# Kernel tuning notes

Measured on AMD Instinct MI355X. Metric: run time of the kernel, lower is better.

Reference implementation:

```python
import jax, jax.numpy as jnp
import numpy as np

B, S, H = 2, 4096, 2048
NH, NKV, HD = 16, 4, 128          # heads, kv heads, head_dim = H // NH
GS_RATIO = 0.25                    # hardcoded in MyAttention.forward
ROPE_BASE = 10000.0


def rotate_half(x):
    h = x.shape[-1] // 2
    return jnp.concatenate((-x[..., h:], x[..., :h]), axis=-1)


def setup_inputs() -> dict:
    key = jax.random.key(0)
    ks = jax.random.split(key, 5)
    g = int(S * GS_RATIO)
    hidden_states = jax.random.normal(ks[0], (B, S, H), jnp.float32)
    position_ids = jnp.tile(jnp.arange(S, dtype=jnp.int32)[None, :], (B, 1))
    # causal additive mask per group window (0 keep, -1e9 masked)
    i = jnp.arange(g)
    causal = i[None, :] <= i[:, None]
    attention_mask = jnp.broadcast_to(
        jnp.where(causal, 0.0, -1e9).astype(jnp.float32)[None, None], (B, 1, g, g)
    )
    sc = 0.02
    Wq = (jax.random.normal(ks[1], (H, NH * HD), jnp.float32) * sc)
    Wk = (jax.random.normal(ks[2], (H, NKV * HD), jnp.float32) * sc)
    Wv = (jax.random.normal(ks[3], (H, NKV * HD), jnp.float32) * sc)
    Wo = (jax.random.normal(ks[4], (NH * HD, H), jnp.float32) * sc)
    return {"hidden_states": hidden_states, "attention_mask": attention_mask,
            "position_ids": position_ids, "Wq": Wq, "Wk": Wk, "Wv": Wv, "Wo": Wo}


def reference(hidden_states, attention_mask, position_ids, Wq, Wk, Wv, Wo):
    B_, S_, H_ = hidden_states.shape
    g = int(S_ * GS_RATIO)
    ng = S_ // g
    n_rep = NH // NKV

    # QKV projections -> (B, heads, S, HD)
    q = (hidden_states @ Wq).reshape(B_, S_, NH, HD).transpose(0, 2, 1, 3)
    k = (hidden_states @ Wk).reshape(B_, S_, NKV, HD).transpose(0, 2, 1, 3)
    v = (hidden_states @ Wv).reshape(B_, S_, NKV, HD).transpose(0, 2, 1, 3)

    # RoPE
    inv_freq = 1.0 / (ROPE_BASE ** (jnp.arange(0, HD, 2, dtype=jnp.float32) / HD))
    t = jnp.arange(S_, dtype=jnp.float32)
    emb = jnp.concatenate([jnp.outer(t, inv_freq)] * 2, axis=-1)  # (S, HD)
    cos = jnp.cos(emb)[position_ids][:, None]  # (B,1,S,HD)
    sin = jnp.sin(emb)[position_ids][:, None]
    q = q * cos + rotate_half(q) * sin
    k = k * cos + rotate_half(k) * sin

    # GQA repeat_kv
    k = jnp.repeat(k, n_rep, axis=1)
    v = jnp.repeat(v, n_rep, axis=1)

    # S2-Attn shift: roll second half of heads by -g/2 along seq, then group
    def shift(x):
        x = jnp.concatenate([x[:, :NH // 2],
                             jnp.roll(x[:, NH // 2:], -g // 2, axis=2)], axis=1)
        return x.transpose(0, 2, 1, 3).reshape(B_ * ng, g, NH, HD).transpose(0, 2, 1, 3)

    q, k, v = shift(q), shift(k), shift(v)

    attn = jnp.einsum('bhqd,bhkd->bhqk', q, k) / np.float32(np.sqrt(HD))
    mask = jnp.tile(attention_mask, (ng, 1, 1, 1))  # (B*ng,1,g,g)
    attn = attn + mask
    attn = jax.nn.softmax(attn.astype(jnp.float32), axis=-1).astype(q.dtype)

    out = jnp.einsum('bhqk,bhkd->bhqd', attn, v)  # (B*ng, NH, g, HD)
    out = out.transpose(0, 2, 1, 3).reshape(B_, S_, NH, HD)
    # undo shift for second half of heads (+g/2 along seq)
    out = jnp.concatenate([out[:, :, :NH // 2],
                           jnp.roll(out[:, :, NH // 2:], g // 2, axis=1)], axis=2)
    out = out.reshape(B_, S_, NH * HD) @ Wo
    return out
```

## Files before the change

kernel.cpp:

```cpp
#include <hip/hip_runtime.h>
#include <math.h>

typedef unsigned short u16;
typedef short bf16x8 __attribute__((ext_vector_type(8)));
typedef float f32x4 __attribute__((ext_vector_type(4)));


__device__ __forceinline__ u16 f2bf(float x) {
  union { float f; unsigned u; } c; c.f = x;
  unsigned r = (c.u + 0x7FFFu + ((c.u >> 16) & 1u)) >> 16;
  return (u16)r;
}
__device__ __forceinline__ float bf2f(u16 x) {
  union { unsigned u; float f; } c; c.u = ((unsigned)x) << 16;
  return c.f;
}

#define GLD16(gp, lp)                                                   \
  __builtin_amdgcn_global_load_lds(                                     \
      (__attribute__((address_space(1))) void*)(gp),                    \
      (__attribute__((address_space(3))) void*)(lp), 16, 0, 0)

#define WAITVM(n) asm volatile("s_waitcnt vmcnt(" #n ")" ::: "memory")
#define LGKM0 { asm volatile("s_waitcnt lgkmcnt(0)" ::: "memory"); \
                __builtin_amdgcn_sched_barrier(0); }
#define BARF  { __builtin_amdgcn_s_barrier(); asm volatile("" ::: "memory"); }

__global__ __launch_bounds__(256) void cast_bf16_vec(
    const float* __restrict__ X, u16* __restrict__ Y) {
  const size_t i = ((size_t)blockIdx.x * 256 + threadIdx.x) * 4;
  float4 v = *(const float4*)(X + i);
  ushort4 o;
  o.x = f2bf(v.x); o.y = f2bf(v.y); o.z = f2bf(v.z); o.w = f2bf(v.w);
  *(ushort4*)(Y + i) = o;
}

__global__ __launch_bounds__(256) void wt_cast(
    const float* __restrict__ W, u16* __restrict__ Wt, int K, int N) {
  const int bk = blockIdx.y * 64;
  const int bn = blockIdx.x * 64;
  __shared__ float T[64 * 65];
  const int tid = threadIdx.x;
  #pragma unroll
  for (int u = 0; u < 16; ++u) {
    int idx = tid + u * 256;
    int kl = idx >> 6, nl = idx & 63;
    T[kl * 65 + nl] = W[(size_t)(bk + kl) * N + bn + nl];
  }
  __syncthreads();
  #pragma unroll
  for (int u = 0; u < 16; ++u) {
    int idx = tid + u * 256;
    int nl = idx >> 6, kl = idx & 63;
    Wt[(size_t)(bn + nl) * K + bk + kl] = f2bf(T[kl * 65 + nl]);
  }
}

__global__ __launch_bounds__(512) void gemm_8ph(
    const u16* __restrict__ A, const u16* __restrict__ Bt,
    float* __restrict__ Cf, u16* __restrict__ Cb, int M, int N, int K) {
  __shared__ u16 As[2][2][8192];
  __shared__ u16 Bs[2][2][8192];

  const int tid = threadIdx.x;

  const int gridN = N >> 8;
  const int nwg = gridDim.x * gridDim.y;
  const int orig = blockIdx.y * gridDim.x + blockIdx.x;
  const int wgid = (orig & 7) * (nwg >> 3) + (orig >> 3);
  const int bm = (wgid / gridN) << 8;
  const int bn = (wgid % gridN) << 8;

  const int w = tid >> 6, lane = tid & 63;
  const int col = lane & 15, quad = lane >> 4;
  const int wm = w >> 2, wn = w & 3;

  const int r0 = tid >> 3;
  const int c0 = tid & 7;
  const int scc8 = ((c0 ^ (r0 & 7)) << 3);
  const u16* aH00 = A  + (size_t)(bm + r0)       * K + scc8;
  const u16* aH01 = A  + (size_t)(bm + 64 + r0)  * K + scc8;
  const u16* aH10 = A  + (size_t)(bm + 128 + r0) * K + scc8;
  const u16* aH11 = A  + (size_t)(bm + 192 + r0) * K + scc8;
  const u16* bH00 = Bt + (size_t)(bn + r0)       * K + scc8;
  const u16* bH01 = Bt + (size_t)(bn + 64 + r0)  * K + scc8;
  const u16* bH10 = Bt + (size_t)(bn + 128 + r0) * K + scc8;
  const u16* bH11 = Bt + (size_t)(bn + 192 + r0) * K + scc8;

#define STG(P0, P1, DST, t_) {                                   \
    GLD16((P0) + (size_t)(t_) * 64, (DST) + tid * 8);            \
    GLD16((P1) + (size_t)(t_) * 64, (DST) + 4096 + tid * 8); }

  const int cx = col & 7;
  const int kc0 = (quad ^ cx) << 3;
  const int kc1 = ((4 + quad) ^ cx) << 3;
  const int arow = (wm * 64 + col) << 6;
  const int brow = (wn * 32 + col) << 6;

  bf16x8 af[4][2], bfr[2][2];
#define RDA(qa, CUR) { _Pragma("unroll") for (int i = 0; i < 4; ++i) {     \
    af[i][0] = *(const bf16x8*)&As[CUR][qa][arow + i * 1024 + kc0];        \
    af[i][1] = *(const bf16x8*)&As[CUR][qa][arow + i * 1024 + kc1]; } }
#define RDB(qb, CUR) { _Pragma("unroll") for (int j = 0; j < 2; ++j) {     \
    bfr[j][0] = *(const bf16x8*)&Bs[CUR][qb][brow + j * 1024 + kc0];       \
    bfr[j][1] = *(const bf16x8*)&Bs[CUR][qb][brow + j * 1024 + kc1]; } }
#define MMA(ACC) { _Pragma("unroll") for (int ks = 0; ks < 2; ++ks)        \
    _Pragma("unroll") for (int i = 0; i < 4; ++i)                          \
    _Pragma("unroll") for (int j = 0; j < 2; ++j)                          \
      ACC[i][j] = __builtin_amdgcn_mfma_f32_16x16x32_bf16(                 \
          af[i][ks], bfr[j][ks], ACC[i][j], 0, 0, 0); }

  f32x4 acc00[4][2], acc01[4][2], acc11[4][2], acc10[4][2];
  #pragma unroll
  for (int i = 0; i < 4; ++i)
    #pragma unroll
    for (int j = 0; j < 2; ++j) {
      acc00[i][j] = (f32x4)(0.0f); acc01[i][j] = (f32x4)(0.0f);
      acc11[i][j] = (f32x4)(0.0f); acc10[i][j] = (f32x4)(0.0f);
    }

  const int NT = K >> 6;

  STG(aH00, aH01, &As[0][0][0], 0);
  STG(bH00, bH01, &Bs[0][0][0], 0);
  STG(bH10, bH11, &Bs[0][1][0], 0);
  STG(aH10, aH11, &As[0][1][0], 0);
  WAITVM(4); BARF;

  for (int t = 0; t < NT - 1; ++t) {
    const int cur = t & 1, nxt = cur ^ 1;

    RDA(0, cur); RDB(0, cur);
    STG(aH00, aH01, &As[nxt][0][0], t + 1);
    LGKM0;
    __builtin_amdgcn_s_setprio(1); MMA(acc00); __builtin_amdgcn_s_setprio(0);
    WAITVM(4); BARF;

    RDB(1, cur);
    STG(bH00, bH01, &Bs[nxt][0][0], t + 1);
    LGKM0;
    __builtin_amdgcn_s_setprio(1); MMA(acc01); __builtin_amdgcn_s_setprio(0);
    WAITVM(4); BARF;

    RDA(1, cur);
    STG(bH10, bH11, &Bs[nxt][1][0], t + 1);
    LGKM0;
    __builtin_amdgcn_s_setprio(1); MMA(acc11); __builtin_amdgcn_s_setprio(0);
    BARF;

    RDB(0, cur);
    STG(aH10, aH11, &As[nxt][1][0], t + 1);
    LGKM0;
    __builtin_amdgcn_s_setprio(1); MMA(acc10); __builtin_amdgcn_s_setprio(0);
    WAITVM(4); BARF;
  }

  {
    const int cur = (NT - 1) & 1;
    RDA(0, cur); RDB(0, cur);
    LGKM0;
    __builtin_amdgcn_s_setprio(1); MMA(acc00); __builtin_amdgcn_s_setprio(0);
    WAITVM(2); BARF;
    RDB(1, cur);
    LGKM0;
    __builtin_amdgcn_s_setprio(1); MMA(acc01); __builtin_amdgcn_s_setprio(0);
    WAITVM(0); BARF;
    RDA(1, cur);
    LGKM0;
    __builtin_amdgcn_s_setprio(1); MMA(acc11); __builtin_amdgcn_s_setprio(0);
    RDB(0, cur);
    LGKM0;
    __builtin_amdgcn_s_setprio(1); MMA(acc10); __builtin_amdgcn_s_setprio(0);
  }

#define WR(ACC, qa, qb) { _Pragma("unroll") for (int i = 0; i < 4; ++i)    \
    _Pragma("unroll") for (int j = 0; j < 2; ++j)                          \
    _Pragma("unroll") for (int r = 0; r < 4; ++r) {                        \
      const int rr = bm + (qa) * 128 + wm * 64 + i * 16 + quad * 4 + r;    \
      const int cc = bn + (qb) * 128 + wn * 32 + j * 16 + col;             \
      if (Cb) Cb[(size_t)rr * N + cc] = f2bf(ACC[i][j][r]);                \
      else    Cf[(size_t)rr * N + cc] = ACC[i][j][r]; } }
  WR(acc00, 0, 0); WR(acc01, 0, 1); WR(acc11, 1, 1); WR(acc10, 1, 0);
#undef WR
#undef RDA
#undef RDB
#undef MMA
#undef STG
}

__global__ __launch_bounds__(256) void rope_qkv(
    u16* __restrict__ QKV, const int* __restrict__ pos) {
  const unsigned idx = blockIdx.x * 256 + threadIdx.x;
  const int d = idx & 63;
  const unsigned rest = idx >> 6;
  const int hh = rest % 20;
  const unsigned bs = rest / 20;

  const int colbase = (hh < 16) ? hh * 128 : 2048 + (hh - 16) * 128;
  u16* p = QKV + (size_t)bs * 3072 + colbase + d;
  const float x0 = bf2f(p[0]);
  const float x1 = bf2f(p[64]);
  const float t = (float)pos[bs];
  const float inv_freq = __expf((float)d * -0.14391156509676332f);
  float s, c;
  __sincosf(t * inv_freq, &s, &c);
  const float sc = (hh < 16) ? 0.08838834764831845f : 1.0f;
  p[0]  = f2bf((x0 * c - x1 * s) * sc);
  p[64] = f2bf((x1 * c + x0 * s) * sc);
}

__global__ __launch_bounds__(256) void v_transpose(
    const u16* __restrict__ QKV, u16* __restrict__ Vt) {
  const int bid = blockIdx.x;
  const int st = bid & 63;
  const int kvh = (bid >> 6) & 3;
  const int b = bid >> 8;
  __shared__ u16 T[64 * 136];
  const int tid = threadIdx.x;
  #pragma unroll
  for (int u = 0; u < 4; ++u) {
    int idx = tid + u * 256;
    int sl = idx >> 4, ch = idx & 15;
    *(uint4*)&T[sl * 136 + ch * 8] =
        *(const uint4*)(QKV + ((size_t)(b * 4096 + st * 64 + sl)) * 3072 + 2560 + kvh * 128 + ch * 8);
  }
  __syncthreads();
  #pragma unroll
  for (int u = 0; u < 32; ++u) {
    int idx = tid + u * 256;
    int d = idx >> 6, sl = idx & 63;
    Vt[((size_t)((b * 4 + kvh) * 128 + d)) * 4096 + st * 64 + sl] = T[sl * 136 + d];
  }
}

__global__ __launch_bounds__(256) void attn_mfma(
    const u16* __restrict__ QKV, const u16* __restrict__ Vt,
    u16* __restrict__ Ob) {
  __shared__ u16 Ks[2][64 * 128];
  __shared__ u16 Vs[2][128 * 64];
  __shared__ u16 Ps[4][16 * 72];

  const int bid = blockIdx.x;
  const int qt = 15 - (bid & 15);
  const int h  = (bid >> 4) & 15;
  const int gi = (bid >> 8) & 3;
  const int b  = bid >> 10;

  const int tid = threadIdx.x;
  const int w = tid >> 6, lane = tid & 63;
  const int col = lane & 15, quad = lane >> 4;

  const int shift = (h >= 8) ? 512 : 0;
  const int base_s = gi * 1024;
  const int kvh = h >> 2;

  const int kco8 = ((tid & 15) ^ ((tid >> 4) & 7)) << 3;
  const int vco8 = ((tid & 7) ^ ((tid >> 3) & 7)) << 3;
  const size_t krow = (size_t)(tid >> 4) * 3072 + kco8;
  const size_t vrow = (size_t)(tid >> 3) * 4096 + vco8;
  u16* kdst = &Ks[0][0] + tid * 8;
  u16* vdst = &Vs[0][0] + tid * 8;
  const size_t vbase = (size_t)((b * 4 + kvh) * 128) * 4096;
  const u16* kgb = QKV + (size_t)b * 4096 * 3072 + 2048 + kvh * 128;

#define ASTAGE(kt_, buf_) {                                               \
    const int sk_ = (base_s + (kt_) * 64 + shift) & 4095;                 \
    const u16* ks_ = kgb + (size_t)sk_ * 3072;                            \
    const u16* vs_ = Vt + vbase + sk_;                                    \
    GLD16(ks_ + krow,             kdst + (buf_) * 8192);                  \
    GLD16(ks_ + krow + 16 * 3072, kdst + (buf_) * 8192 + 2048);           \
    GLD16(ks_ + krow + 32 * 3072, kdst + (buf_) * 8192 + 4096);           \
    GLD16(ks_ + krow + 48 * 3072, kdst + (buf_) * 8192 + 6144);           \
    GLD16(vs_ + vrow,             vdst + (buf_) * 8192);                  \
    GLD16(vs_ + vrow + 32 * 4096, vdst + (buf_) * 8192 + 2048);           \
    GLD16(vs_ + vrow + 64 * 4096, vdst + (buf_) * 8192 + 4096);           \
    GLD16(vs_ + vrow + 96 * 4096, vdst + (buf_) * 8192 + 6144);           \
  }

  const int sq0 = (base_s + qt * 64 + shift) & 4095;
  {
    const u16* qsrc = QKV + ((size_t)(b * 4096 + sq0)) * 3072 + h * 128;
    GLD16(qsrc + krow,             kdst);
    GLD16(qsrc + krow + 16 * 3072, kdst + 2048);
    GLD16(qsrc + krow + 32 * 3072, kdst + 4096);
    GLD16(qsrc + krow + 48 * 3072, kdst + 6144);
  }
  asm volatile("s_waitcnt vmcnt(0)" ::: "memory");
  __builtin_amdgcn_s_barrier();
  asm volatile("" ::: "memory");

  const int cxor = col & 7;
  bf16x8 aq[4];
  {
    const int qr = w * 16 + col;
    #pragma unroll
    for (int kk = 0; kk < 4; ++kk)
      aq[kk] = *(const bf16x8*)&Ks[0][qr * 128 + ((((kk << 2) + quad) ^ cxor) << 3)];
  }
  asm volatile("s_waitcnt lgkmcnt(0)" ::: "memory");
  __builtin_amdgcn_s_barrier();
  asm volatile("" ::: "memory");

  ASTAGE(0, 0);

  f32x4 o[8];
  #pragma unroll
  for (int jd = 0; jd < 8; ++jd) o[jd] = (f32x4)(0.0f);
  float lp[4] = {0.0f, 0.0f, 0.0f, 0.0f};

  u16* Pw = &Ps[w][0];
  const int qrow_l = w * 16 + quad * 4;

  for (int kt = 0; kt <= qt; ++kt) {
    const u16* Kc = &Ks[kt & 1][0];
    const u16* Vc = &Vs[kt & 1][0];
    const bool pf = (kt < qt);
    if (pf) ASTAGE(kt + 1, (kt + 1) & 1);
    if (pf) asm volatile("s_waitcnt vmcnt(8)" ::: "memory");
    else    asm volatile("s_waitcnt vmcnt(0)" ::: "memory");
    __builtin_amdgcn_s_barrier();
    asm volatile("" ::: "memory");

    f32x4 scv[4];
    #pragma unroll
    for (int j = 0; j < 4; ++j) scv[j] = (f32x4)(0.0f);
    __builtin_amdgcn_s_setprio(1);
    #pragma unroll
    for (int kk = 0; kk < 4; ++kk) {
      #pragma unroll
      for (int j = 0; j < 4; ++j) {
        bf16x8 bk = *(const bf16x8*)&Kc[(16 * j + col) * 128 + ((((kk << 2) + quad) ^ cxor) << 3)];
        scv[j] = __builtin_amdgcn_mfma_f32_16x16x32_bf16(aq[kk], bk, scv[j], 0, 0, 0);
      }
    }
    __builtin_amdgcn_s_setprio(0);

    const bool last = (kt == qt);
    #pragma unroll
    for (int j = 0; j < 4; ++j) {
      #pragma unroll
      for (int r = 0; r < 4; ++r) {
        float p = __expf(scv[j][r]);
        if (last && (16 * j + col) > (qrow_l + r)) p = 0.0f;
        lp[r] += p;
        Pw[(quad * 4 + r) * 72 + 16 * j + col] = f2bf(p);
      }
    }

    __builtin_amdgcn_s_setprio(1);
    #pragma unroll
    for (int ks = 0; ks < 2; ++ks) {
      bf16x8 ap = *(const bf16x8*)&Pw[col * 72 + ks * 32 + quad * 8];
      #pragma unroll
      for (int jd = 0; jd < 8; ++jd) {
        bf16x8 bv = *(const bf16x8*)&Vc[(16 * jd + col) * 64 + ((((ks << 2) + quad) ^ cxor) << 3)];
        o[jd] = __builtin_amdgcn_mfma_f32_16x16x32_bf16(ap, bv, o[jd], 0, 0, 0);
      }
    }
    __builtin_amdgcn_s_setprio(0);

    asm volatile("" ::: "memory");
    __builtin_amdgcn_s_barrier();
  }
#undef ASTAGE

  #pragma unroll
  for (int r = 0; r < 4; ++r) {
    lp[r] += __shfl_xor(lp[r], 1, 64);
    lp[r] += __shfl_xor(lp[r], 2, 64);
    lp[r] += __shfl_xor(lp[r], 4, 64);
    lp[r] += __shfl_xor(lp[r], 8, 64);
  }

  #pragma unroll
  for (int r = 0; r < 4; ++r) {
    const int qg = qt * 64 + w * 16 + quad * 4 + r;
    const int sq = (base_s + qg + shift) & 4095;
    u16* dst = Ob + ((size_t)(b * 4096 + sq)) * 2048 + h * 128;
    const float inv = 1.0f / lp[r];
    #pragma unroll
    for (int jd = 0; jd < 8; ++jd)
      dst[16 * jd + col] = f2bf(o[jd][r] * inv);
  }
}

extern "C" void kernel_launch(void* const* d_in, const int* in_sizes, int n_in,
                              void* d_out, int out_size, void* d_ws, size_t ws_size,
                              hipStream_t stream) {
  const float* hs = (const float*)d_in[0];
  const int*   pos = (const int*)d_in[2];
  const float* Wq = (const float*)d_in[3];
  const float* Wk = (const float*)d_in[4];
  const float* Wv = (const float*)d_in[5];
  const float* Wo = (const float*)d_in[6];

  char* ws = (char*)d_ws;
  u16* hsb   = (u16*)ws; ws += (size_t)8192 * 2048 * 2;
  u16* Wqkvt = (u16*)ws; ws += (size_t)3072 * 2048 * 2;
  u16* Wot   = (u16*)ws; ws += (size_t)2048 * 2048 * 2;
  u16* QKVb  = (u16*)ws; ws += (size_t)8192 * 3072 * 2;
  u16* Vtt   = (u16*)ws; ws += (size_t)2 * 4 * 128 * 4096 * 2;
  u16* Obh   = (u16*)ws; ws += (size_t)8192 * 2048 * 2;

  dim3 blk(256);

  cast_bf16_vec<<<16384, blk, 0, stream>>>(hs, hsb);
  wt_cast<<<dim3(32, 32), blk, 0, stream>>>(Wq, Wqkvt, 2048, 2048);
  wt_cast<<<dim3(8, 32),  blk, 0, stream>>>(Wk, Wqkvt + (size_t)2048 * 2048, 2048, 512);
  wt_cast<<<dim3(8, 32),  blk, 0, stream>>>(Wv, Wqkvt + (size_t)2560 * 2048, 2048, 512);
  wt_cast<<<dim3(32, 32), blk, 0, stream>>>(Wo, Wot, 2048, 2048);

  gemm_8ph<<<dim3(12, 32), dim3(512), 0, stream>>>(hsb, Wqkvt, nullptr, QKVb, 8192, 3072, 2048);

  rope_qkv<<<40960, blk, 0, stream>>>(QKVb, pos);

  v_transpose<<<512, blk, 0, stream>>>(QKVb, Vtt);

  attn_mfma<<<2048, blk, 0, stream>>>(QKVb, Vtt, Obh);

  gemm_8ph<<<dim3(8, 32), dim3(512), 0, stream>>>(Obh, Wot, (float*)d_out, nullptr, 8192, 2048, 2048);
}
```

Baseline: 496.4 us.

## Replace 4-phase GEMM schedule with single-barrier per K-tile flow

The hand-scheduled 8-phase GEMM main loop, with four barriers per K-tile and explicit lgkmcnt waits and sched_barriers, is replaced by a simpler loop. Each iteration issues all four next-tile global→LDS loads up front, then reads A and both B fragments and runs all four MMA quadrants with fragment reuse, and ends with one vmcnt(0) wait plus one barrier. The aim is to cut barrier and synchronisation overhead and let the compiler schedule LDS reads against MFMAs. In exchange it gives up the fine-grained overlap of the phased schedule and uses more live fragment registers.

```diff
diff --git a/kernel.cpp b/kernel.cpp
--- a/kernel.cpp
+++ b/kernel.cpp
@@ -22,8 +22,6 @@
       (__attribute__((address_space(3))) void*)(lp), 16, 0, 0)
 
 #define WAITVM(n) asm volatile("s_waitcnt vmcnt(" #n ")" ::: "memory")
-#define LGKM0 { asm volatile("s_waitcnt lgkmcnt(0)" ::: "memory"); \
-                __builtin_amdgcn_sched_barrier(0); }
 #define BARF  { __builtin_amdgcn_s_barrier(); asm volatile("" ::: "memory"); }
 
 __global__ __launch_bounds__(256) void cast_bf16_vec(
@@ -56,7 +54,7 @@
   }
 }
 
-__global__ __launch_bounds__(512) void gemm_8ph(
+__global__ __launch_bounds__(512) void gemm_flow(
     const u16* __restrict__ A, const u16* __restrict__ Bt,
     float* __restrict__ Cf, u16* __restrict__ Cb, int M, int N, int K) {
   __shared__ u16 As[2][2][8192];
@@ -97,18 +95,17 @@
   const int arow = (wm * 64 + col) << 6;
   const int brow = (wn * 32 + col) << 6;
 
-  bf16x8 af[4][2], bfr[2][2];
-#define RDA(qa, CUR) { _Pragma("unroll") for (int i = 0; i < 4; ++i) {     \
-    af[i][0] = *(const bf16x8*)&As[CUR][qa][arow + i * 1024 + kc0];        \
-    af[i][1] = *(const bf16x8*)&As[CUR][qa][arow + i * 1024 + kc1]; } }
-#define RDB(qb, CUR) { _Pragma("unroll") for (int j = 0; j < 2; ++j) {     \
-    bfr[j][0] = *(const bf16x8*)&Bs[CUR][qb][brow + j * 1024 + kc0];       \
-    bfr[j][1] = *(const bf16x8*)&Bs[CUR][qb][brow + j * 1024 + kc1]; } }
-#define MMA(ACC) { _Pragma("unroll") for (int ks = 0; ks < 2; ++ks)        \
-    _Pragma("unroll") for (int i = 0; i < 4; ++i)                          \
-    _Pragma("unroll") for (int j = 0; j < 2; ++j)                          \
-      ACC[i][j] = __builtin_amdgcn_mfma_f32_16x16x32_bf16(                 \
-          af[i][ks], bfr[j][ks], ACC[i][j], 0, 0, 0); }
+#define RDA(DST, qa, CUR) { _Pragma("unroll") for (int i = 0; i < 4; ++i) { \
+    DST[i][0] = *(const bf16x8*)&As[CUR][qa][arow + i * 1024 + kc0];        \
+    DST[i][1] = *(const bf16x8*)&As[CUR][qa][arow + i * 1024 + kc1]; } }
+#define RDB(DST, qb, CUR) { _Pragma("unroll") for (int j = 0; j < 2; ++j) { \
+    DST[j][0] = *(const bf16x8*)&Bs[CUR][qb][brow + j * 1024 + kc0];        \
+    DST[j][1] = *(const bf16x8*)&Bs[CUR][qb][brow + j * 1024 + kc1]; } }
+#define MMA(ACC, AF, BF) { _Pragma("unroll") for (int ks = 0; ks < 2; ++ks) \
+    _Pragma("unroll") for (int i = 0; i < 4; ++i)                           \
+    _Pragma("unroll") for (int j = 0; j < 2; ++j)                           \
+      ACC[i][j] = __builtin_amdgcn_mfma_f32_16x16x32_bf16(                  \
+          AF[i][ks], BF[j][ks], ACC[i][j], 0, 0, 0); }
 
   f32x4 acc00[4][2], acc01[4][2], acc11[4][2], acc10[4][2];
   #pragma unroll
@@ -125,52 +122,34 @@
   STG(bH00, bH01, &Bs[0][0][0], 0);
   STG(bH10, bH11, &Bs[0][1][0], 0);
   STG(aH10, aH11, &As[0][1][0], 0);
-  WAITVM(4); BARF;
-
-  for (int t = 0; t < NT - 1; ++t) {
+  WAITVM(0); BARF;
+
+  for (int t = 0; t < NT; ++t) {
     const int cur = t & 1, nxt = cur ^ 1;
 
-    RDA(0, cur); RDB(0, cur);
-    STG(aH00, aH01, &As[nxt][0][0], t + 1);
-    LGKM0;
-    __builtin_amdgcn_s_setprio(1); MMA(acc00); __builtin_amdgcn_s_setprio(0);
-    WAITVM(4); BARF;
-
-    RDB(1, cur);
-    STG(bH00, bH01, &Bs[nxt][0][0], t + 1);
-    LGKM0;
-    __builtin_amdgcn_s_setprio(1); MMA(acc01); __builtin_amdgcn_s_setprio(0);
-    WAITVM(4); BARF;
-
-    RDA(1, cur);
-    STG(bH10, bH11, &Bs[nxt][1][0], t + 1);
-    LGKM0;
-    __builtin_amdgcn_s_setprio(1); MMA(acc11); __builtin_amdgcn_s_setprio(0);
+    if (t + 1 < NT) {
+      STG(aH00, aH01, &As[nxt][0][0], t + 1);
+      STG(bH00, bH01, &Bs[nxt][0][0], t + 1);
+      STG(bH10, bH11, &Bs[nxt][1][0], t + 1);
+      STG(aH10, aH11, &As[nxt][1][0], t + 1);
+    }
+
+    {
+      bf16x8 af[4][2], b0[2][2], b1[2][2];
+      RDA(af, 0, cur); RDB(b0, 0, cur); RDB(b1, 1, cur);
+      __builtin_amdgcn_s_setprio(1);
+      MMA(acc00, af, b0);
+      MMA(acc01, af, b1);
+      __builtin_amdgcn_s_setprio(0);
+      RDA(af, 1, cur);
+      __builtin_amdgcn_s_setprio(1);
+      MMA(acc11, af, b1);
+      MMA(acc10, af, b0);
+      __builtin_amdgcn_s_setprio(0);
+    }
+
+    if (t + 1 < NT) WAITVM(0);
     BARF;
-
-    RDB(0, cur);
-    STG(aH10, aH11, &As[nxt][1][0], t + 1);
-    LGKM0;
-    __builtin_amdgcn_s_setprio(1); MMA(acc10); __builtin_amdgcn_s_setprio(0);
-    WAITVM(4); BARF;
-  }
-
-  {
-    const int cur = (NT - 1) & 1;
-    RDA(0, cur); RDB(0, cur);
-    LGKM0;
-    __builtin_amdgcn_s_setprio(1); MMA(acc00); __builtin_amdgcn_s_setprio(0);
-    WAITVM(2); BARF;
-    RDB(1, cur);
-    LGKM0;
-    __builtin_amdgcn_s_setprio(1); MMA(acc01); __builtin_amdgcn_s_setprio(0);
-    WAITVM(0); BARF;
-    RDA(1, cur);
-    LGKM0;
-    __builtin_amdgcn_s_setprio(1); MMA(acc11); __builtin_amdgcn_s_setprio(0);
-    RDB(0, cur);
-    LGKM0;
-    __builtin_amdgcn_s_setprio(1); MMA(acc10); __builtin_amdgcn_s_setprio(0);
   }
 
 #define WR(ACC, qa, qb) { _Pragma("unroll") for (int i = 0; i < 4; ++i)    \
@@ -410,7 +389,7 @@
   wt_cast<<<dim3(8, 32),  blk, 0, stream>>>(Wv, Wqkvt + (size_t)2560 * 2048, 2048, 512);
   wt_cast<<<dim3(32, 32), blk, 0, stream>>>(Wo, Wot, 2048, 2048);
 
-  gemm_8ph<<<dim3(12, 32), dim3(512), 0, stream>>>(hsb, Wqkvt, nullptr, QKVb, 8192, 3072, 2048);
+  gemm_flow<<<dim3(12, 32), dim3(512), 0, stream>>>(hsb, Wqkvt, nullptr, QKVb, 8192, 3072, 2048);
 
   rope_qkv<<<40960, blk, 0, stream>>>(QKVb, pos);
 
@@ -418,5 +397,5 @@
 
   attn_mfma<<<2048, blk, 0, stream>>>(QKVb, Vtt, Obh);
 
-  gemm_8ph<<<dim3(8, 32), dim3(512), 0, stream>>>(Obh, Wot, (float*)d_out, nullptr, 8192, 2048, 2048);
-}
+  gemm_flow<<<dim3(8, 32), dim3(512), 0, stream>>>(Obh, Wot, (float*)d_out, nullptr, 8192, 2048, 2048);
+}
```

After: 508.1 us. 2.4% more time.
